# Optimization experiments

Measured on AMD Instinct MI355X. Metric: run time of the kernel, lower is better.

Reference implementation:

```python
import jax, jax.numpy as jnp
import numpy as np

N, M, E = 100000, 500, 300000
XS, GS, OUT, HEADS = 100, 100, 100, 2
SLOPE = 0.2
EPS = 1e-12


def l2norm(x, axis):
    n = jnp.linalg.norm(x, axis=axis, keepdims=True)
    return x / jnp.maximum(n, EPS)


def gat_layer(h_ijk, ends, n, W, att):
    # W: [heads*out, in_dim] (no bias); att: [1, heads, out]
    heads, out = att.shape[1], att.shape[2]
    c = (h_ijk @ W.T).reshape(-1, heads, out)               # [E, H, D]
    a = jnp.sum(att * c, axis=2, keepdims=True)             # [E, H, 1]
    e = jnp.exp(-jax.nn.leaky_relu(a, SLOPE))
    denom = jax.ops.segment_sum(e, ends, num_segments=n)    # [n, H, 1]
    alpha = e / denom[ends]                                 # segment softmax (dropout=eval/identity)
    h = jax.ops.segment_sum(alpha * c, ends, num_segments=n)  # [n, H, D]
    h = jax.nn.elu(h)
    h = l2norm(h, axis=2)
    return h.reshape(n, heads * out)


def merge_layer(h_in, h_out, Wi, bi, Wo, bo, Wl, bl):
    hi = h_in @ Wi.T + bi
    ho = h_out @ Wo.T + bo
    lam = jax.nn.sigmoid(jnp.concatenate([hi, ho], axis=1) @ Wl.T + bl)
    h = lam * hi + (1.0 - lam) * ho
    return l2norm(jax.nn.elu(h), axis=1)


def setup_inputs() -> dict:
    key = jax.random.key(0)
    ks = jax.random.split(key, 24)
    D = HEADS * OUT  # 200
    in1 = 2 * XS + GS   # 300
    in2 = 3 * D         # 600
    s = 0.05
    return {
        'edge_idx': jax.random.randint(ks[0], (2, E), 0, N),
        'edge_type': jax.random.randint(ks[1], (E,), 0, M),
        'path_idx': jax.random.randint(ks[2], (2, 8), 0, N),
        'path_type': jax.random.randint(ks[3], (2, 8), 0, M),
        'use_path': 0,
        'x': jax.random.normal(ks[4], (N, XS), jnp.float32),
        'g': jax.random.normal(ks[5], (M, GS), jnp.float32),
        'W_in1': s * jax.random.normal(ks[6], (D, in1), jnp.float32),
        'att_in1': s * jax.random.normal(ks[7], (1, HEADS, OUT), jnp.float32),
        'W_out1': s * jax.random.normal(ks[8], (D, in1), jnp.float32),
        'att_out1': s * jax.random.normal(ks[9], (1, HEADS, OUT), jnp.float32),
        'Wi1': s * jax.random.normal(ks[10], (D, D), jnp.float32), 'bi1': jnp.zeros((D,), jnp.float32),
        'Wo1': s * jax.random.normal(ks[11], (D, D), jnp.float32), 'bo1': jnp.zeros((D,), jnp.float32),
        'Wl1': s * jax.random.normal(ks[12], (1, 2 * D), jnp.float32), 'bl1': jnp.zeros((1,), jnp.float32),
        'Wr': s * jax.random.normal(ks[13], (D, GS), jnp.float32), 'br': jnp.zeros((D,), jnp.float32),
        'Wf': s * jax.random.normal(ks[14], (D, in1), jnp.float32), 'bf': jnp.zeros((D,), jnp.float32),
        'W_in2': s * jax.random.normal(ks[15], (D, in2), jnp.float32),
        'att_in2': s * jax.random.normal(ks[16], (1, 1, D), jnp.float32),
        'W_out2': s * jax.random.normal(ks[17], (D, in2), jnp.float32),
        'att_out2': s * jax.random.normal(ks[18], (1, 1, D), jnp.float32),
        'Wi2': s * jax.random.normal(ks[19], (D, D), jnp.float32), 'bi2': jnp.zeros((D,), jnp.float32),
        'Wo2': s * jax.random.normal(ks[20], (D, D), jnp.float32), 'bo2': jnp.zeros((D,), jnp.float32),
        'Wl2': s * jax.random.normal(ks[21], (1, 2 * D), jnp.float32), 'bl2': jnp.zeros((1,), jnp.float32),
        'W_ent': s * jax.random.normal(ks[22], (D, XS), jnp.float32),
    }


def reference(edge_idx, edge_type, path_idx, path_type, use_path, x, g,
              W_in1, att_in1, W_out1, att_out1, Wi1, bi1, Wo1, bo1, Wl1, bl1,
              Wr, br, Wf, bf,
              W_in2, att_in2, W_out2, att_out2, Wi2, bi2, Wo2, bo2, Wl2, bl2,
              W_ent):
    n, m = x.shape[0], g.shape[0]
    x = l2norm(x, axis=1)  # x_initial is renormalized each forward
    row, col = edge_idx[0], edge_idx[1]
    # hop 1: gather-concat per-edge features [E, 2*XS+GS]
    h_ijk = jnp.concatenate([x[row], x[col], g[edge_type]], axis=1)
    h_in = gat_layer(h_ijk, col, n, W_in1, att_in1)
    h_out = gat_layer(h_ijk, row, n, W_out1, att_out1)
    h = merge_layer(h_in, h_out, Wi1, bi1, Wo1, bo1, Wl1, bl1)
    # relation layer
    g_edges = jax.ops.segment_sum(h_ijk, edge_type, num_segments=m)
    g_edges = jax.nn.elu(l2norm(g_edges, axis=1))
    g_prime = (g @ Wr.T + br) + (g_edges @ Wf.T + bf)
    # hop 2
    h_ijk2 = jnp.concatenate([h[row], h[col], g_prime[edge_type]], axis=1)
    h_in2 = gat_layer(h_ijk2, col, n, W_in2, att_in2)
    h_out2 = gat_layer(h_ijk2, row, n, W_out2, att_out2)
    h = merge_layer(h_in2, h_out2, Wi2, bi2, Wo2, bo2, Wl2, bl2)
    # entity residual layer
    h_prime = x @ W_ent.T + h
    return h_prime
```

## Files before the change

### kernel.cpp

```cpp
#include <hip/hip_runtime.h>
#include <cstddef>
#include <cstdint>

#define WSLOPE 0.2f
#define WEPS 1e-12f

typedef __attribute__((ext_vector_type(8))) short bf16x8;
typedef __attribute__((ext_vector_type(4))) float f32x4;

__device__ __forceinline__ float waveSum(float v) {
#pragma unroll
    for (int off = 32; off > 0; off >>= 1) v += __shfl_xor(v, off, 64);
    return v;
}
__device__ __forceinline__ float eluf(float v) { return v > 0.f ? v : expm1f(v); }
__device__ __forceinline__ short f2bf(float f) {
    union { float f; uint32_t u; } v; v.f = f;
    uint32_t r = v.u + 0x7FFF + ((v.u >> 16) & 1);
    return (short)(r >> 16);
}

__global__ void k_invnorm(const float* __restrict__ x, float* __restrict__ invn, int N) {
    int wid = blockIdx.x * 4 + (threadIdx.x >> 6);
    int lane = threadIdx.x & 63;
    if (wid >= N) return;
    const float* p = x + (size_t)wid * 100;
    float a = p[lane];
    float ss = a * a;
    if (lane < 36) { float b = p[lane + 64]; ss += b * b; }
    ss = waveSum(ss);
    if (lane == 0) invn[wid] = 1.f / fmaxf(sqrtf(ss), WEPS);
}

__global__ void k_count(const int* __restrict__ keys, int* __restrict__ cnt, int n) {
    int i = blockIdx.x * 256 + threadIdx.x;
    if (i < n) atomicAdd(&cnt[keys[i]], 1);
}

#define SCAN_CHUNK 2048
__global__ void k_blocksum(const int* __restrict__ cnt, int* __restrict__ bsum, int n) {
    __shared__ int sh[256];
    int b = blockIdx.x, t = threadIdx.x;
    int base = b * SCAN_CHUNK;
    int s = 0;
    for (int i = t; i < SCAN_CHUNK; i += 256) { int idx = base + i; if (idx < n) s += cnt[idx]; }
    sh[t] = s; __syncthreads();
    for (int off = 128; off > 0; off >>= 1) { if (t < off) sh[t] += sh[t + off]; __syncthreads(); }
    if (t == 0) bsum[b] = sh[0];
}

__global__ void k_scanwrite(const int* __restrict__ cnt, const int* __restrict__ bsum,
                            int* __restrict__ offs, int* __restrict__ cur, int n, int nb) {
    __shared__ int sh[256];
    __shared__ int sbase;
    int b = blockIdx.x, t = threadIdx.x;
    if (t == 0) { int s = 0; for (int i = 0; i < b; ++i) s += bsum[i]; sbase = s; }
    __syncthreads();
    int base = b * SCAN_CHUNK;
    int loc[8]; int ts = 0;
#pragma unroll
    for (int i = 0; i < 8; ++i) { int idx = base + t * 8 + i; int v = (idx < n) ? cnt[idx] : 0; loc[i] = ts; ts += v; }
    sh[t] = ts; __syncthreads();
    for (int off = 1; off < 256; off <<= 1) {
        int v = (t >= off) ? sh[t - off] : 0;
        __syncthreads();
        sh[t] += v;
        __syncthreads();
    }
    int excl = (t == 0) ? 0 : sh[t - 1];
    int gbase = sbase + excl;
#pragma unroll
    for (int i = 0; i < 8; ++i) {
// ... 44 lines not shown
    int wid = blockIdx.x * 4 + (threadIdx.x >> 6);
    int lane = threadIdx.x & 63;
    if (wid >= N) return;
    if (!HOP2) {
        float inv = invn[wid];
        const float* p = feat + (size_t)wid * 100;
        float f0 = p[lane] * inv;
        float f1 = (lane < 36) ? p[lane + 64] * inv : 0.f;
#pragma unroll
        for (int h = 0; h < 2; ++h) {
            const float* w = wa + h * 300;
            float r = f0 * w[lane] + ((lane < 36) ? f1 * w[lane + 64] : 0.f);
            float c = f0 * w[100 + lane] + ((lane < 36) ? f1 * w[100 + lane + 64] : 0.f);
            r = waveSum(r); c = waveSum(c);
            if (lane == 0) { rdot[wid * 2 + h] = r; cdot[wid * 2 + h] = c; }
        }
    } else {
        const float* p = feat + (size_t)wid * 200;
        float r = 0.f, c = 0.f;
#pragma unroll
        for (int m = 0; m < 4; ++m) {
            int d = lane + m * 64;
            if (d < 200) { float f = p[d]; r += f * wa[d]; c += f * wa[200 + d]; }
        }
        r = waveSum(r); c = waveSum(c);
        if (lane == 0) { rdot[wid] = r; cdot[wid] = c; }
    }
}

__global__ void k_gdot(const float* __restrict__ gsrc, const float* __restrict__ wa,
                       float* __restrict__ gdot, int M, int H, int GL, int K) {
    int id = blockIdx.x * 256 + threadIdx.x;
    if (id >= M * H) return;
    int m = id / H, h = id % H;
    float s = 0.f;
    const float* w = wa + h * K + 2 * GL;
    const float* gm = gsrc + (size_t)m * GL;
    for (int kk = 0; kk < GL; ++kk) s += gm[kk] * w[kk];
    gdot[id] = s;
}

__global__ void k_ew_s(const int* __restrict__ nbrS, const int* __restrict__ keyS,
                       const int* __restrict__ etS,
                       const float* __restrict__ ndot, const float* __restrict__ kdot,
                       const float* __restrict__ gdot, float* __restrict__ ewS, int E, int H) {
    int id = blockIdx.x * 256 + threadIdx.x;
    if (id >= E * H) return;
    int p = id / H, h = id - p * H;
    float a = ndot[nbrS[p] * H + h] + kdot[keyS[p] * H + h] + gdot[etS[p] * H + h];
    float lr = a > 0.f ? a : WSLOPE * a;
    ewS[id] = expf(-lr);
}

template<int H, bool HOP2>
__global__ void k_agg(const int* __restrict__ offs, const int* __restrict__ nbrS,
                      const int* __restrict__ etS, const float* __restrict__ ewS,
                      const float* __restrict__ projg,
                      const float* __restrict__ feat, const float* __restrict__ invn,
                      short* __restrict__ agg_b, float* __restrict__ hb, int n0, int n1) {
    int node = n0 + blockIdx.x * 4 + (threadIdx.x >> 6);
    int lane = threadIdx.x & 63;
    if (node >= n1) return;
    int o = offs[node];
    int deg = offs[node + 1] - o;
    float va[7];
#pragma unroll
    for (int m = 0; m < 7; ++m) va[m] = 0.f;
    if (deg > 0) {
        float s0 = 0.f, s1 = 0.f;
        for (int i = lane; i < deg; i += 64) {
            s0 += ewS[(size_t)(o + i) * H];
            if (H == 2) s1 += ewS[(size_t)(o + i) * H + 1];
        }
        s0 = waveSum(s0);
        float rd0 = 1.f / s0, rd1 = rd0;
        if (H == 2) { s1 = waveSum(s1); rd1 = 1.f / s1; }
        for (int j = 0; j < deg; ++j) {
            float a0 = ewS[(size_t)(o + j) * H] * rd0;
            float a1 = (H == 2) ? ewS[(size_t)(o + j) * H + 1] * rd1 : a0;
            int nbr = nbrS[o + j];
            int et = etS[o + j];
            const float* pgr = projg + (size_t)et * 200;
            if (!HOP2) {
                float inv = invn[nbr];
                const float* fr = feat + (size_t)nbr * 100;
#pragma unroll
                for (int m = 0; m < 7; ++m) {
                    int d = lane + m * 64;
                    if (d < 200) {
                        int kk = d >= 100 ? d - 100 : d;
                        float al = d < 100 ? a0 : a1;
                        va[m] += al * fr[kk] * inv;
                    } else if (d < 400) {
                        int dd = d - 200;
                        float al = dd < 100 ? a0 : a1;
                        va[m] += al * pgr[dd];
                    }
                }
            } else {
                const float* fr = feat + (size_t)nbr * 200;
#pragma unroll
                for (int m = 0; m < 7; ++m) {
                    int d = lane + m * 64;
                    if (d < 200) va[m] += a0 * fr[d];
                    else if (d < 400) va[m] += a0 * pgr[d - 200];
                }
            }
        }
    }
    size_t rb = (size_t)(node - n0);
#pragma unroll
    for (int m = 0; m < 7; ++m) {
        int d = lane + m * 64;
        if (d < 200) {
            int slot = HOP2 ? d : (d < 100 ? d : d + 12);
            agg_b[rb * 224 + slot] = f2bf(va[m]);
        } else if (d < 400) {
            hb[rb * 200 + (d - 200)] = va[m];
        }
    }
    if (!HOP2) {
        if (lane < 24) { int s = lane < 12 ? 100 + lane : 200 + lane; agg_b[rb * 224 + s] = 0; }
    } else {
        if (lane < 24) agg_b[rb * 224 + 200 + lane] = 0;
    }
}

template<int KSTEPS, bool BIAS, bool ACC, bool DEGMASK>
__launch_bounds__(256)
__global__ void k_mgemm(const short* __restrict__ A, const short* __restrict__ Wb,
                        const float* __restrict__ bias, const int* __restrict__ degoffs,
                        float* __restrict__ out, int rows, int lda) {
    constexpr int LDW = KSTEPS * 32;
    const int t = threadIdx.x;
    const int wv = t >> 6, l = t & 63;
    const int lhi = l >> 4, llo = l & 15;
    const int rbase = blockIdx.x * 64 + wv * 16;
    f32x4 acc[13];
#pragma unroll
    for (int j = 0; j < 13; ++j) acc[j] = f32x4{0.f, 0.f, 0.f, 0.f};
    const short* arow = A + (size_t)(rbase + llo) * lda + lhi * 8;
#pragma unroll
    for (int kt = 0; kt < KSTEPS; ++kt) {
        bf16x8 a = *(const bf16x8*)(arow + kt * 32);
#pragma unroll
        for (int j = 0; j < 13; ++j) {
            bf16x8 b = *(const bf16x8*)(Wb + (size_t)(j * 16 + llo) * LDW + kt * 32 + lhi * 8);
            acc[j] = __builtin_amdgcn_mfma_f32_16x16x32_bf16(a, b, acc[j], 0, 0, 0);
        }
    }
    const int r0 = rbase + lhi * 4;
#pragma unroll
    for (int e = 0; e < 4; ++e) {
        int r = r0 + e;
        if (r >= rows) continue;
        float dm = 1.f;
        if (DEGMASK) dm = (degoffs[r + 1] - degoffs[r] == 0) ? 0.f : 1.f;
        float* orow = out + (size_t)r * 200;
#pragma unroll
        for (int j = 0; j < 13; ++j) {
            int d = j * 16 + llo;
            if (d < 200) {
                float v = acc[j][e] * dm;
                if (BIAS) v += bias[d];
                if (ACC) v += orow[d];
                orow[d] = v;
            }
        }
    }
}

__global__ void k_prepw(const float* __restrict__ W, int ldW, int koff, int Klen, int Kpad,
                        int mode, short* __restrict__ Wb) {
    int id = blockIdx.x * 256 + threadIdx.x;
    int tot = 208 * Kpad;
    if (id >= tot) return;
    int d = id / Kpad, k = id - d * Kpad;
    float v = 0.f;
    if (d < 200) {
        if (mode == 0) { if (k < Klen) v = W[(size_t)d * ldW + koff + k]; }
        else { int h = d / 100; int kk = k - h * 112; if (kk >= 0 && kk < 100) v = W[(size_t)d * ldW + koff + kk]; }
    }
    Wb[id] = f2bf(v);
}

__global__ void k_prepwrf(const float* __restrict__ Wr, const float* __restrict__ Wf,
                          short* __restrict__ Wb) {
    int id = blockIdx.x * 256 + threadIdx.x;
    if (id >= 208 * 448) return;
    int d = id / 448, k = id - d * 448;
    float v = 0.f;
    if (d < 200) {
        if (k < 100) v = Wr[(size_t)d * 100 + k];
        else if (k >= 128 && k < 428) v = Wf[(size_t)d * 300 + (k - 128)];
    }
    Wb[id] = f2bf(v);
}

__global__ void k_brf(const float* __restrict__ br, const float* __restrict__ bf,
                      float* __restrict__ brf) {
    int d = threadIdx.x;
    if (d < 200) brf[d] = br[d] + bf[d];
}

__global__ void k_xcb(const float* __restrict__ x, const float* __restrict__ invn,
                      short* __restrict__ sb, int rows) {
    int id = blockIdx.x * 256 + threadIdx.x;
    if (id >= rows * 128) return;
    int r = id >> 7, k = id & 127;
    sb[id] = f2bf(k < 100 ? x[(size_t)r * 100 + k] * invn[r] : 0.f);
}

__global__ void k_gcb(const float* __restrict__ g, short* __restrict__ gb, int rows) {
    int id = blockIdx.x * 256 + threadIdx.x;
    if (id >= rows * 128) return;
    int r = id >> 7, k = id & 127;
    gb[(size_t)r * 448 + k] = f2bf(k < 100 ? g[(size_t)r * 100 + k] : 0.f);
}

__global__ void k_h1b(const float* __restrict__ h1, short* __restrict__ sb, int rows) {
    int id = blockIdx.x * 256 + threadIdx.x;
    if (id >= rows * 224) return;
    int r = id / 224, k = id - r * 224;
    sb[id] = f2bf(k < 200 ? h1[(size_t)r * 200 + k] : 0.f);
}

template<int DH, int H>
__global__ void gat_post2(const float* __restrict__ hb, short* __restrict__ pb, int rowsH) {
    int nh = blockIdx.x * 4 + (threadIdx.x >> 6);
    int lane = threadIdx.x & 63;
    if (nh >= rowsH) return;
    const float* p = hb + (size_t)nh * DH;
    constexpr int MM = (DH + 63) / 64;
    float v[MM];
    float ss = 0.f;
#pragma unroll
    for (int m = 0; m < MM; ++m) {
        int d = lane + m * 64;
        v[m] = 0.f;
        if (d < DH) { v[m] = eluf(p[d]); ss += v[m] * v[m]; }
    }
    ss = waveSum(ss);
    float inv = 1.f / fmaxf(sqrtf(ss), WEPS);
    short* ob = pb + (size_t)(nh / H) * 224 + (size_t)(nh % H) * DH;
#pragma unroll
    for (int m = 0; m < MM; ++m) {
        int d = lane + m * 64;
        if (d < DH) ob[d] = f2bf(v[m] * inv);
    }
}

__global__ void merge_comb(const float* __restrict__ hi, const float* __restrict__ ho,
                           const float* __restrict__ Wl, const float* __restrict__ bl,
                           float* __restrict__ out, int N) {
    int wid = blockIdx.x * 4 + (threadIdx.x >> 6);
    int lane = threadIdx.x & 63;
    if (wid >= N) return;
    float vi[4], vo[4];
    float s = 0.f;
#pragma unroll
    for (int m = 0; m < 4; ++m) {
        int d = lane + m * 64;
        vi[m] = 0.f; vo[m] = 0.f;
        if (d < 200) {
            vi[m] = hi[(size_t)wid * 200 + d];
            vo[m] = ho[(size_t)wid * 200 + d];
            s += Wl[d] * vi[m] + Wl[200 + d] * vo[m];
        }
    }
    s = waveSum(s);
    float lam = 1.f / (1.f + expf(-(s + bl[0])));
    float hv[4];
    float ss = 0.f;
#pragma unroll
    for (int m = 0; m < 4; ++m) {
        int d = lane + m * 64;
        hv[m] = 0.f;
        if (d < 200) {
            float h = lam * vi[m] + (1.f - lam) * vo[m];
            hv[m] = eluf(h);
            ss += hv[m] * hv[m];
        }
    }
    ss = waveSum(ss);
    float inv = 1.f / fmaxf(sqrtf(ss), WEPS);
#pragma unroll
    for (int m = 0; m < 4; ++m) {
        int d = lane + m * 64;
        if (d < 200) out[(size_t)wid * 200 + d] = hv[m] * inv;
    }
}

__global__ void k_gedges_b(const int* __restrict__ rsT, const int* __restrict__ csT,
                           const int* __restrict__ offsT,
                           const float* __restrict__ x, const float* __restrict__ invn,
                           const float* __restrict__ g, short* __restrict__ gcomb, int M) {
    __shared__ float red[4];
    int m = blockIdx.x, t = threadIdx.x;
    int o = offsT[m];
    int deg = offsT[m + 1] - o;
    float acc = 0.f;
    if (t < 100) {
        for (int i = 0; i < deg; ++i) {
            int r = rsT[o + i];
            acc += x[(size_t)r * 100 + t] * invn[r];
        }
    } else if (t < 200) {
        for (int i = 0; i < deg; ++i) {
            int c = csT[o + i];
            acc += x[(size_t)c * 100 + (t - 100)] * invn[c];
        }
    }
    float gval = 0.f;
    if (t < 100) gval = (float)deg * g[(size_t)m * 100 + t];
    float sq = acc * acc + gval * gval;
    sq = waveSum(sq);
    if ((t & 63) == 0) red[t >> 6] = sq;
    __syncthreads();
    float s2 = red[0] + red[1] + red[2] + red[3];
    float inv = 1.f / fmaxf(sqrtf(s2), WEPS);
    short* orow = gcomb + (size_t)m * 448 + 128;
    if (t < 200) orow[t] = f2bf(eluf(acc * inv));
    if (t < 100) orow[200 + t] = f2bf(eluf(gval * inv));
    if (t >= 200 && t < 220) orow[100 + t] = 0;
}

extern "C" void kernel_launch(void* const* d_in, const int* in_sizes, int n_in,
                              void* d_out, int out_size, void* d_ws, size_t ws_size,
                              hipStream_t stream) {
    const int* eidx   = (const int*)d_in[0];
    const int* etype  = (const int*)d_in[1];
    const float* x    = (const float*)d_in[5];
    const float* g    = (const float*)d_in[6];
    const float* W_in1  = (const float*)d_in[7];
    const float* att_in1 = (const float*)d_in[8];
    const float* W_out1 = (const float*)d_in[9];
    const float* att_out1 = (const float*)d_in[10];
    const float* Wi1 = (const float*)d_in[11]; const float* bi1 = (const float*)d_in[12];
    const float* Wo1 = (const float*)d_in[13]; const float* bo1 = (const float*)d_in[14];
    const float* Wl1 = (const float*)d_in[15]; const float* bl1 = (const float*)d_in[16];
    const float* Wr  = (const float*)d_in[17]; const float* br  = (const float*)d_in[18];
    const float* Wf  = (const float*)d_in[19]; const float* bf  = (const float*)d_in[20];
    const float* W_in2  = (const float*)d_in[21]; const float* att_in2 = (const float*)d_in[22];
    const float* W_out2 = (const float*)d_in[23]; const float* att_out2 = (const float*)d_in[24];
    const float* Wi2 = (const float*)d_in[25]; const float* bi2 = (const float*)d_in[26];
    const float* Wo2 = (const float*)d_in[27]; const float* bo2 = (const float*)d_in[28];
    const float* Wl2 = (const float*)d_in[29]; const float* bl2 = (const float*)d_in[30];
    const float* W_ent = (const float*)d_in[31];

    const int E = in_sizes[1];
    const int N = in_sizes[5] / 100;
    const int M = in_sizes[6] / 100;
    const int Mr = (M + 63) & ~63;
    float* out = (float*)d_out;
    const int* row = eidx;
    const int* col = eidx + E;

    char* w = (char*)d_ws;
    size_t off_b = 0;
    auto alloc = [&](size_t bytes) -> void* {
        void* p = w + off_b;
        off_b += (bytes + 255) & ~(size_t)255;
        return p;
    };
    float* invn  = (float*)alloc((size_t)N * 4);
    float* h1    = (float*)alloc((size_t)N * 200 * 4);
    int* offs_in = (int*)alloc((size_t)(N + 1) * 4);
    int* offs_out= (int*)alloc((size_t)(N + 1) * 4);
    int* offsT   = (int*)alloc((size_t)(M + 1) * 4);
    int* nbrS_in = (int*)alloc((size_t)E * 4);
    int* etS_in  = (int*)alloc((size_t)E * 4);
    int* keyS_in = (int*)alloc((size_t)E * 4);
    int* nbrS_out= (int*)alloc((size_t)E * 4);
    int* etS_out = (int*)alloc((size_t)E * 4);
    int* keyS_out= (int*)alloc((size_t)E * 4);
    int* rsT     = (int*)alloc((size_t)E * 4);
    int* csT     = (int*)alloc((size_t)E * 4);
    int* cnt     = (int*)alloc((size_t)N * 4);
    int* cur     = (int*)alloc((size_t)N * 4);
    int* bsum    = (int*)alloc((size_t)64 * 4);
    float* wa_in = (float*)alloc((size_t)1200 * 4);
    float* wa_out= (float*)alloc((size_t)1200 * 4);
    float* rdot_in = (float*)alloc((size_t)N * 2 * 4);
    float* cdot_in = (float*)alloc((size_t)N * 2 * 4);
    float* rdot_out= (float*)alloc((size_t)N * 2 * 4);
    float* cdot_out= (float*)alloc((size_t)N * 2 * 4);
    float* gdot_in = (float*)alloc((size_t)M * 2 * 4);
    float* gdot_out= (float*)alloc((size_t)M * 2 * 4);
    float* ewS_in  = (float*)alloc((size_t)E * 2 * 4);
    float* ewS_out = (float*)alloc((size_t)E * 2 * 4);
    float* pg_in   = (float*)alloc((size_t)M * 200 * 4);
    float* pg_out  = (float*)alloc((size_t)M * 200 * 4);
    float* gp      = (float*)alloc((size_t)M * 200 * 4);
    short* gcomb   = (short*)alloc((size_t)Mr * 448 * 2);
    short* Ws_in1  = (short*)alloc((size_t)208 * 128 * 2);
    short* Ws_out1 = (short*)alloc((size_t)208 * 128 * 2);
    short* Wa_in1  = (short*)alloc((size_t)208 * 224 * 2);
    short* Wa_out1 = (short*)alloc((size_t)208 * 224 * 2);
    short* Wm_i1   = (short*)alloc((size_t)208 * 224 * 2);
    short* Wm_o1   = (short*)alloc((size_t)208 * 224 * 2);
    short* Ws_in2  = (short*)alloc((size_t)208 * 224 * 2);
    short* Ws_out2 = (short*)alloc((size_t)208 * 224 * 2);
    short* Wa_in2  = (short*)alloc((size_t)208 * 224 * 2);
    short* Wa_out2 = (short*)alloc((size_t)208 * 224 * 2);
    short* Wm_i2   = (short*)alloc((size_t)208 * 224 * 2);
    short* Wm_o2   = (short*)alloc((size_t)208 * 224 * 2);
    short* Wb_ent  = (short*)alloc((size_t)208 * 128 * 2);
    short* Wg_in1  = (short*)alloc((size_t)208 * 128 * 2);
    short* Wg_out1 = (short*)alloc((size_t)208 * 128 * 2);
    short* Wg_in2  = (short*)alloc((size_t)208 * 224 * 2);
    short* Wg_out2 = (short*)alloc((size_t)208 * 224 * 2);
    short* Wrf_b   = (short*)alloc((size_t)208 * 448 * 2);
    float* brf     = (float*)alloc((size_t)200 * 4);

    if (off_b >= ws_size) return;
    size_t rem = ws_size - off_b;
    long long Cll = (long long)(rem / 3072);
    long long Nr64 = ((long long)N + 63) & ~63LL;
    int C = (int)(Cll > Nr64 ? Nr64 : Cll);
    C &= ~63;
    if (C < 64) return;
    float* hbA   = (float*)alloc((size_t)C * 200 * 4);
    float* hbB   = (float*)alloc((size_t)C * 200 * 4);
    short* agg_b = (short*)alloc((size_t)C * 224 * 2);
    short* post_b= (short*)alloc((size_t)C * 224 * 2);
    short* sb    = (short*)alloc((size_t)C * 224 * 2);
    if (off_b > ws_size) return;

    const int gE = (E + 255) / 256;
    const int gN4 = (N + 3) / 4;
    const int gM64 = (M + 63) / 64;

    k_invnorm<<<gN4, 256, 0, stream>>>(x, invn, N);

    hipMemsetAsync(post_b, 0, (size_t)C * 224 * 2, stream);

    const int gW224 = (208 * 224 + 255) / 256;
    const int gW128 = (208 * 128 + 255) / 256;
    const int gW448 = (208 * 448 + 255) / 256;
    k_prepw<<<gW128, 256, 0, stream>>>(W_in1, 300, 100, 100, 128, 0, Ws_in1);
    k_prepw<<<gW128, 256, 0, stream>>>(W_out1, 300, 0, 100, 128, 0, Ws_out1);
    k_prepw<<<gW224, 256, 0, stream>>>(W_in1, 300, 0, 100, 224, 1, Wa_in1);
    k_prepw<<<gW224, 256, 0, stream>>>(W_out1, 300, 100, 100, 224, 1, Wa_out1);
    k_prepw<<<gW224, 256, 0, stream>>>(Wi1, 200, 0, 200, 224, 0, Wm_i1);
    k_prepw<<<gW224, 256, 0, stream>>>(Wo1, 200, 0, 200, 224, 0, Wm_o1);
    k_prepw<<<gW224, 256, 0, stream>>>(W_in2, 600, 200, 200, 224, 0, Ws_in2);
    k_prepw<<<gW224, 256, 0, stream>>>(W_out2, 600, 0, 200, 224, 0, Ws_out2);
    k_prepw<<<gW224, 256, 0, stream>>>(W_in2, 600, 0, 200, 224, 0, Wa_in2);
    k_prepw<<<gW224, 256, 0, stream>>>(W_out2, 600, 200, 200, 224, 0, Wa_out2);
    k_prepw<<<gW224, 256, 0, stream>>>(Wi2, 200, 0, 200, 224, 0, Wm_i2);
    k_prepw<<<gW224, 256, 0, stream>>>(Wo2, 200, 0, 200, 224, 0, Wm_o2);
    k_prepw<<<gW128, 256, 0, stream>>>(W_ent, 100, 0, 100, 128, 0, Wb_ent);
    k_prepw<<<gW128, 256, 0, stream>>>(W_in1, 300, 200, 100, 128, 0, Wg_in1);
    k_prepw<<<gW128, 256, 0, stream>>>(W_out1, 300, 200, 100, 128, 0, Wg_out1);
    k_prepw<<<gW224, 256, 0, stream>>>(W_in2, 600, 400, 200, 224, 0, Wg_in2);
    k_prepw<<<gW224, 256, 0, stream>>>(W_out2, 600, 400, 200, 224, 0, Wg_out2);
    k_prepwrf<<<gW448, 256, 0, stream>>>(Wr, Wf, Wrf_b);
    k_brf<<<1, 256, 0, stream>>>(br, bf, brf);

    int nbN = (N + SCAN_CHUNK - 1) / SCAN_CHUNK;
    int nbM = (M + SCAN_CHUNK - 1) / SCAN_CHUNK;
    hipMemsetAsync(cnt, 0, (size_t)N * 4, stream);
    k_count<<<gE, 256, 0, stream>>>(col, cnt, E);
    k_blocksum<<<nbN, 256, 0, stream>>>(cnt, bsum, N);
    k_scanwrite<<<nbN, 256, 0, stream>>>(cnt, bsum, offs_in, cur, N, nbN);
    k_scatter3<<<gE, 256, 0, stream>>>(col, row, etype, cur, nbrS_in, etS_in, keyS_in, E);

    hipMemsetAsync(cnt, 0, (size_t)N * 4, stream);
    k_count<<<gE, 256, 0, stream>>>(row, cnt, E);
    k_blocksum<<<nbN, 256, 0, stream>>>(cnt, bsum, N);
    k_scanwrite<<<nbN, 256, 0, stream>>>(cnt, bsum, offs_out, cur, N, nbN);
    k_scatter3<<<gE, 256, 0, stream>>>(row, col, etype, cur, nbrS_out, etS_out, keyS_out, E);

    hipMemsetAsync(cnt, 0, (size_t)M * 4, stream);
    k_count<<<gE, 256, 0, stream>>>(etype, cnt, E);
    k_blocksum<<<nbM, 256, 0, stream>>>(cnt, bsum, M);
    k_scanwrite<<<nbM, 256, 0, stream>>>(cnt, bsum, offsT, cur, M, nbM);
    k_scatter2<<<gE, 256, 0, stream>>>(etype, cur, rsT, csT, row, col, E);

    k_watt<<<(2 * 300 + 255) / 256, 256, 0, stream>>>(att_in1, W_in1, wa_in, 2, 100, 300);
    k_watt<<<(2 * 300 + 255) / 256, 256, 0, stream>>>(att_out1, W_out1, wa_out, 2, 100, 300);
    k_dots<false><<<gN4, 256, 0, stream>>>(x, invn, wa_in, rdot_in, cdot_in, N);
    k_dots<false><<<gN4, 256, 0, stream>>>(x, invn, wa_out, rdot_out, cdot_out, N);
    k_gdot<<<(M * 2 + 255) / 256, 256, 0, stream>>>(g, wa_in, gdot_in, M, 2, 100, 300);
    k_gdot<<<(M * 2 + 255) / 256, 256, 0, stream>>>(g, wa_out, gdot_out, M, 2, 100, 300);
    k_gcb<<<((int)(((size_t)M * 128 + 255) / 256)), 256, 0, stream>>>(g, gcomb, M);
    k_mgemm<4, false, false, false><<<gM64, 256, 0, stream>>>(gcomb, Wg_in1, nullptr, nullptr, pg_in, M, 448);
    k_mgemm<4, false, false, false><<<gM64, 256, 0, stream>>>(gcomb, Wg_out1, nullptr, nullptr, pg_out, M, 448);
    k_ew_s<<<(E * 2 + 255) / 256, 256, 0, stream>>>(nbrS_in, keyS_in, etS_in, rdot_in, cdot_in, gdot_in, ewS_in, E, 2);
    k_ew_s<<<(E * 2 + 255) / 256, 256, 0, stream>>>(nbrS_out, keyS_out, etS_out, cdot_out, rdot_out, gdot_out, ewS_out, E, 2);

    for (int n0 = 0; n0 < N; n0 += C) {
        int rows = (N - n0 < C) ? (N - n0) : C;
        int n1 = n0 + rows;
        int ga = (rows + 3) / 4;
        int gb = (rows + 63) / 64;
        k_xcb<<<(rows * 128 + 255) / 256, 256, 0, stream>>>(x + (size_t)n0 * 100, invn + n0, sb, rows);
        k_agg<2, false><<<ga, 256, 0, stream>>>(offs_in, nbrS_in, etS_in, ewS_in, pg_in, x, invn, agg_b, hbA, n0, n1);
        k_mgemm<4, false, true, true><<<gb, 256, 0, stream>>>(sb, Ws_in1, nullptr, offs_in + n0, hbA, rows, 128);
        k_mgemm<7, false, true, false><<<gb, 256, 0, stream>>>(agg_b, Wa_in1, nullptr, nullptr, hbA, rows, 224);
        k_agg<2, false><<<ga, 256, 0, stream>>>(offs_out, nbrS_out, etS_out, ewS_out, pg_out, x, invn, agg_b, hbB, n0, n1);
        k_mgemm<4, false, true, true><<<gb, 256, 0, stream>>>(sb, Ws_out1, nullptr, offs_out + n0, hbB, rows, 128);
        k_mgemm<7, false, true, false><<<gb, 256, 0, stream>>>(agg_b, Wa_out1, nullptr, nullptr, hbB, rows, 224);
        gat_post2<100, 2><<<(2 * rows + 3) / 4, 256, 0, stream>>>(hbA, post_b, 2 * rows);
        k_mgemm<7, true, false, false><<<gb, 256, 0, stream>>>(post_b, Wm_i1, bi1, nullptr, hbA, rows, 224);
        gat_post2<100, 2><<<(2 * rows + 3) / 4, 256, 0, stream>>>(hbB, post_b, 2 * rows);
        k_mgemm<7, true, false, false><<<gb, 256, 0, stream>>>(post_b, Wm_o1, bo1, nullptr, hbB, rows, 224);
        merge_comb<<<ga, 256, 0, stream>>>(hbA, hbB, Wl1, bl1, h1 + (size_t)n0 * 200, rows);
    }

    k_gedges_b<<<M, 256, 0, stream>>>(rsT, csT, offsT, x, invn, g, gcomb, M);
    k_mgemm<14, true, false, false><<<gM64, 256, 0, stream>>>(gcomb, Wrf_b, brf, nullptr, gp, M, 448);

    k_watt<<<(600 + 255) / 256, 256, 0, stream>>>(att_in2, W_in2, wa_in, 1, 200, 600);
    k_watt<<<(600 + 255) / 256, 256, 0, stream>>>(att_out2, W_out2, wa_out, 1, 200, 600);
    k_dots<true><<<gN4, 256, 0, stream>>>(h1, nullptr, wa_in, rdot_in, cdot_in, N);
    k_dots<true><<<gN4, 256, 0, stream>>>(h1, nullptr, wa_out, rdot_out, cdot_out, N);
    k_gdot<<<(M + 255) / 256, 256, 0, stream>>>(gp, wa_in, gdot_in, M, 1, 200, 600);
    k_gdot<<<(M + 255) / 256, 256, 0, stream>>>(gp, wa_out, gdot_out, M, 1, 200, 600);
    k_h1b<<<((int)(((size_t)M * 224 + 255) / 256)), 256, 0, stream>>>(gp, gcomb, M);
    k_mgemm<7, false, false, false><<<gM64, 256, 0, stream>>>(gcomb, Wg_in2, nullptr, nullptr, pg_in, M, 224);
    k_mgemm<7, false, false, false><<<gM64, 256, 0, stream>>>(gcomb, Wg_out2, nullptr, nullptr, pg_out, M, 224);
    k_ew_s<<<(E + 255) / 256, 256, 0, stream>>>(nbrS_in, keyS_in, etS_in, rdot_in, cdot_in, gdot_in, ewS_in, E, 1);
    k_ew_s<<<(E + 255) / 256, 256, 0, stream>>>(nbrS_out, keyS_out, etS_out, cdot_out, rdot_out, gdot_out, ewS_out, E, 1);

    for (int n0 = 0; n0 < N; n0 += C) {
        int rows = (N - n0 < C) ? (N - n0) : C;
        int n1 = n0 + rows;
        int ga = (rows + 3) / 4;
        int gb = (rows + 63) / 64;
        k_h1b<<<(rows * 224 + 255) / 256, 256, 0, stream>>>(h1 + (size_t)n0 * 200, sb, rows);
        k_agg<1, true><<<ga, 256, 0, stream>>>(offs_in, nbrS_in, etS_in, ewS_in, pg_in, h1, nullptr, agg_b, hbA, n0, n1);
        k_mgemm<7, false, true, true><<<gb, 256, 0, stream>>>(sb, Ws_in2, nullptr, offs_in + n0, hbA, rows, 224);
        k_mgemm<7, false, true, false><<<gb, 256, 0, stream>>>(agg_b, Wa_in2, nullptr, nullptr, hbA, rows, 224);
        k_agg<1, true><<<ga, 256, 0, stream>>>(offs_out, nbrS_out, etS_out, ewS_out, pg_out, h1, nullptr, agg_b, hbB, n0, n1);
        k_mgemm<7, false, true, true><<<gb, 256, 0, stream>>>(sb, Ws_out2, nullptr, offs_out + n0, hbB, rows, 224);
        k_mgemm<7, false, true, false><<<gb, 256, 0, stream>>>(agg_b, Wa_out2, nullptr, nullptr, hbB, rows, 224);
        gat_post2<200, 1><<<ga, 256, 0, stream>>>(hbA, post_b, rows);
        k_mgemm<7, true, false, false><<<gb, 256, 0, stream>>>(post_b, Wm_i2, bi2, nullptr, hbA, rows, 224);
        gat_post2<200, 1><<<ga, 256, 0, stream>>>(hbB, post_b, rows);
        k_mgemm<7, true, false, false><<<gb, 256, 0, stream>>>(post_b, Wm_o2, bo2, nullptr, hbB, rows, 224);
        merge_comb<<<ga, 256, 0, stream>>>(hbA, hbB, Wl2, bl2, out + (size_t)n0 * 200, rows);
        k_xcb<<<(rows * 128 + 255) / 256, 256, 0, stream>>>(x + (size_t)n0 * 100, invn + n0, sb, rows);
        k_mgemm<4, false, true, false><<<gb, 256, 0, stream>>>(sb, Wb_ent, nullptr, nullptr, out + (size_t)n0 * 200, rows, 128);
    }
}
```

Before: 2.958 ms.

## Fuse GAT projections into single concatenated-K GEMM over bf16 aggregated features

The aggregation kernel now gathers bf16 node and relation features, skipping the per-relation projected tables, and writes one wide A row per node holding the aggregated node features, aggregated relation features and the masked self features. A single MFMA GEMM with concatenated weights (K=576 or 672) then replaces the three separate GEMMs and the relation pre-projection GEMMs. Node features are pre-converted to bf16 once, and merge_comb emits a bf16 copy of h1 for hop 2. This removes several kernel launches and repeated fp32 read-modify-write passes over the output buffers. In exchange it adds more bf16 rounding of gathered features and a larger per-row A buffer, which shrinks the chunk size.

```diff
diff --git a/kernel.cpp b/kernel.cpp
--- a/kernel.cpp
+++ b/kernel.cpp
@@ -18,6 +18,10 @@
     union { float f; uint32_t u; } v; v.f = f;
     uint32_t r = v.u + 0x7FFF + ((v.u >> 16) & 1);
     return (short)(r >> 16);
+}
+__device__ __forceinline__ float bf2f(short s) {
+    union { uint32_t u; float f; } v; v.u = ((uint32_t)(uint16_t)s) << 16;
+    return v.f;
 }
 
 __global__ void k_invnorm(const float* __restrict__ x, float* __restrict__ invn, int N) {
@@ -168,12 +172,15 @@
     ewS[id] = expf(-lr);
 }
 
-template<int H, bool HOP2>
+template<bool HOP2>
 __global__ void k_agg(const int* __restrict__ offs, const int* __restrict__ nbrS,
                       const int* __restrict__ etS, const float* __restrict__ ewS,
-                      const float* __restrict__ projg,
-                      const float* __restrict__ feat, const float* __restrict__ invn,
-                      short* __restrict__ agg_b, float* __restrict__ hb, int n0, int n1) {
+                      const short* __restrict__ featB, const short* __restrict__ gB,
+                      short* __restrict__ A, int n0, int n1) {
+    constexpr int H = HOP2 ? 1 : 2;
+    constexpr int LDA = HOP2 ? 672 : 576;
+    constexpr int FW = HOP2 ? 224 : 112;
+    constexpr int GW = HOP2 ? 224 : 112;
     int node = n0 + blockIdx.x * 4 + (threadIdx.x >> 6);
     int lane = threadIdx.x & 63;
     if (node >= n1) return;
@@ -196,56 +203,65 @@
             float a1 = (H == 2) ? ewS[(size_t)(o + j) * H + 1] * rd1 : a0;
             int nbr = nbrS[o + j];
             int et = etS[o + j];
-            const float* pgr = projg + (size_t)et * 200;
+            const short* fr = featB + (size_t)nbr * FW;
+            const short* gr = gB + (size_t)et * GW;
             if (!HOP2) {
-                float inv = invn[nbr];
-                const float* fr = feat + (size_t)nbr * 100;
 #pragma unroll
                 for (int m = 0; m < 7; ++m) {
                     int d = lane + m * 64;
-                    if (d < 200) {
-                        int kk = d >= 100 ? d - 100 : d;
-                        float al = d < 100 ? a0 : a1;
-                        va[m] += al * fr[kk] * inv;
-                    } else if (d < 400) {
-                        int dd = d - 200;
-                        float al = dd < 100 ? a0 : a1;
-                        va[m] += al * pgr[dd];
-                    }
+                    if (d < 100) va[m] += a0 * bf2f(fr[d]);
+                    else if (d < 200) va[m] += a1 * bf2f(fr[d - 100]);
+                    else if (d < 300) va[m] += a0 * bf2f(gr[d - 200]);
+                    else if (d < 400) va[m] += a1 * bf2f(gr[d - 300]);
                 }
             } else {
-                const float* fr = feat + (size_t)nbr * 200;
 #pragma unroll
                 for (int m = 0; m < 7; ++m) {
                     int d = lane + m * 64;
-                    if (d < 200) va[m] += a0 * fr[d];
-                    else if (d < 400) va[m] += a0 * pgr[d - 200];
+                    if (d < 200) va[m] += a0 * bf2f(fr[d]);
+                    else if (d < 424) va[m] += a0 * bf2f(gr[d - 200]);
                 }
             }
         }
     }
     size_t rb = (size_t)(node - n0);
-#pragma unroll
-    for (int m = 0; m < 7; ++m) {
-        int d = lane + m * 64;
-        if (d < 200) {
-            int slot = HOP2 ? d : (d < 100 ? d : d + 12);
-            agg_b[rb * 224 + slot] = f2bf(va[m]);
-        } else if (d < 400) {
-            hb[rb * 200 + (d - 200)] = va[m];
-        }
-    }
+    short* Ar = A + rb * LDA;
     if (!HOP2) {
-        if (lane < 24) { int s = lane < 12 ? 100 + lane : 200 + lane; agg_b[rb * 224 + s] = 0; }
+#pragma unroll
+        for (int m = 0; m < 7; ++m) {
+            int d = lane + m * 64;
+            if (d < 400) {
+                int col = d < 100 ? d : (d < 200 ? d + 12 : (d < 300 ? d + 24 : d + 36));
+                Ar[col] = f2bf(va[m]);
+            }
+        }
+        if (lane < 48) { int q = lane / 12; int rm = lane - q * 12; Ar[q * 112 + 100 + rm] = 0; }
+        const short* sf = featB + (size_t)node * 112;
+#pragma unroll
+        for (int mm = 0; mm < 2; ++mm) {
+            int k = lane + mm * 64;
+            if (k < 128) Ar[448 + k] = (deg > 0 && k < 112) ? sf[k] : (short)0;
+        }
     } else {
-        if (lane < 24) agg_b[rb * 224 + 200 + lane] = 0;
-    }
-}
-
-template<int KSTEPS, bool BIAS, bool ACC, bool DEGMASK>
+#pragma unroll
+        for (int m = 0; m < 7; ++m) {
+            int d = lane + m * 64;
+            if (d < 424) Ar[d < 200 ? d : d + 24] = f2bf(va[m]);
+        }
+        if (lane < 24) Ar[200 + lane] = 0;
+        const short* sf = featB + (size_t)node * 224;
+#pragma unroll
+        for (int mm = 0; mm < 4; ++mm) {
+            int k = lane + mm * 64;
+            if (k < 224) Ar[448 + k] = deg > 0 ? sf[k] : (short)0;
+        }
+    }
+}
+
+template<int KSTEPS, bool BIAS, bool ACC>
 __launch_bounds__(256)
 __global__ void k_mgemm(const short* __restrict__ A, const short* __restrict__ Wb,
-                        const float* __restrict__ bias, const int* __restrict__ degoffs,
+                        const float* __restrict__ bias,
                         float* __restrict__ out, int rows, int lda) {
     constexpr int LDW = KSTEPS * 32;
     const int t = threadIdx.x;
@@ -270,14 +286,12 @@
     for (int e = 0; e < 4; ++e) {
         int r = r0 + e;
         if (r >= rows) continue;
-        float dm = 1.f;
-        if (DEGMASK) dm = (degoffs[r + 1] - degoffs[r] == 0) ? 0.f : 1.f;
         float* orow = out + (size_t)r * 200;
 #pragma unroll
         for (int j = 0; j < 13; ++j) {
             int d = j * 16 + llo;
             if (d < 200) {
-                float v = acc[j][e] * dm;
+                float v = acc[j][e];
                 if (BIAS) v += bias[d];
                 if (ACC) v += orow[d];
                 orow[d] = v;
@@ -286,18 +300,18 @@
     }
 }
 
-__global__ void k_prepw(const float* __restrict__ W, int ldW, int koff, int Klen, int Kpad,
-                        int mode, short* __restrict__ Wb) {
-    int id = blockIdx.x * 256 + threadIdx.x;
-    int tot = 208 * Kpad;
+__global__ void k_prepw(const float* __restrict__ W, int ldW, int koff, int Klen, int span,
+                        int mode, short* __restrict__ Wb, int ldWb, int dst) {
+    int id = blockIdx.x * 256 + threadIdx.x;
+    int tot = 208 * span;
     if (id >= tot) return;
-    int d = id / Kpad, k = id - d * Kpad;
+    int d = id / span, k = id - d * span;
     float v = 0.f;
     if (d < 200) {
         if (mode == 0) { if (k < Klen) v = W[(size_t)d * ldW + koff + k]; }
-        else { int h = d / 100; int kk = k - h * 112; if (kk >= 0 && kk < 100) v = W[(size_t)d * ldW + koff + kk]; }
-    }
-    Wb[id] = f2bf(v);
+        else { int h = d / 100; int kk = k - h * 112; if (kk >= 0 && kk < Klen) v = W[(size_t)d * ldW + koff + kk]; }
+    }
+    Wb[(size_t)d * ldWb + dst + k] = f2bf(v);
 }
 
 __global__ void k_prepwrf(const float* __restrict__ Wr, const float* __restrict__ Wf,
@@ -319,12 +333,14 @@
     if (d < 200) brf[d] = br[d] + bf[d];
 }
 
-__global__ void k_xcb(const float* __restrict__ x, const float* __restrict__ invn,
-                      short* __restrict__ sb, int rows) {
-    int id = blockIdx.x * 256 + threadIdx.x;
-    if (id >= rows * 128) return;
-    int r = id >> 7, k = id & 127;
-    sb[id] = f2bf(k < 100 ? x[(size_t)r * 100 + k] * invn[r] : 0.f);
+__global__ void k_cvt112(const float* __restrict__ src, const float* __restrict__ invn,
+                         short* __restrict__ dst, int rows) {
+    int id = blockIdx.x * 256 + threadIdx.x;
+    if (id >= rows * 112) return;
+    int r = id / 112, k = id - r * 112;
+    float v = 0.f;
+    if (k < 100) { v = src[(size_t)r * 100 + k]; if (invn) v *= invn[r]; }
+    dst[id] = f2bf(v);
 }
 
 __global__ void k_gcb(const float* __restrict__ g, short* __restrict__ gb, int rows) {
@@ -368,7 +384,7 @@
 
 __global__ void merge_comb(const float* __restrict__ hi, const float* __restrict__ ho,
                            const float* __restrict__ Wl, const float* __restrict__ bl,
-                           float* __restrict__ out, int N) {
+                           float* __restrict__ out, short* __restrict__ hbf, int N) {
     int wid = blockIdx.x * 4 + (threadIdx.x >> 6);
     int lane = threadIdx.x & 63;
     if (wid >= N) return;
@@ -403,7 +419,13 @@
 #pragma unroll
     for (int m = 0; m < 4; ++m) {
         int d = lane + m * 64;
-        if (d < 200) out[(size_t)wid * 200 + d] = hv[m] * inv;
+        if (d < 200) {
+            float v = hv[m] * inv;
+            out[(size_t)wid * 200 + d] = v;
+            if (hbf) hbf[(size_t)wid * 224 + d] = f2bf(v);
+        } else if (d < 224) {
+            if (hbf) hbf[(size_t)wid * 224 + d] = 0;
+        }
     }
 }
 
@@ -411,34 +433,43 @@
                            const int* __restrict__ offsT,
                            const float* __restrict__ x, const float* __restrict__ invn,
                            const float* __restrict__ g, short* __restrict__ gcomb, int M) {
-    __shared__ float red[4];
+    __shared__ float red[6];
     int m = blockIdx.x, t = threadIdx.x;
     int o = offsT[m];
     int deg = offsT[m + 1] - o;
     float acc = 0.f;
-    if (t < 100) {
+    if (t < 128) {
+        int d = t; bool ok = d < 100;
         for (int i = 0; i < deg; ++i) {
             int r = rsT[o + i];
-            acc += x[(size_t)r * 100 + t] * invn[r];
-        }
-    } else if (t < 200) {
+            if (ok) acc += x[(size_t)r * 100 + d] * invn[r];
+        }
+    } else if (t < 256) {
+        int d = t - 128; bool ok = d < 100;
         for (int i = 0; i < deg; ++i) {
             int c = csT[o + i];
-            acc += x[(size_t)c * 100 + (t - 100)] * invn[c];
-        }
-    }
-    float gval = 0.f;
-    if (t < 100) gval = (float)deg * g[(size_t)m * 100 + t];
-    float sq = acc * acc + gval * gval;
-    sq = waveSum(sq);
+            if (ok) acc += x[(size_t)c * 100 + d] * invn[c];
+        }
+    } else {
+        int d = t - 256;
+        if (d < 100) acc = (float)deg * g[(size_t)m * 100 + d];
+    }
+    float sq = waveSum(acc * acc);
     if ((t & 63) == 0) red[t >> 6] = sq;
     __syncthreads();
-    float s2 = red[0] + red[1] + red[2] + red[3];
+    float s2 = red[0] + red[1] + red[2] + red[3] + red[4] + red[5];
     float inv = 1.f / fmaxf(sqrtf(s2), WEPS);
     short* orow = gcomb + (size_t)m * 448 + 128;
-    if (t < 200) orow[t] = f2bf(eluf(acc * inv));
-    if (t < 100) orow[200 + t] = f2bf(eluf(gval * inv));
-    if (t >= 200 && t < 220) orow[100 + t] = 0;
+    if (t < 128) {
+        if (t < 100) orow[t] = f2bf(eluf(acc * inv));
+    } else if (t < 256) {
+        int d = t - 128;
+        if (d < 100) orow[100 + d] = f2bf(eluf(acc * inv));
+    } else {
+        int d = t - 256;
+        if (d < 100) orow[200 + d] = f2bf(eluf(acc * inv));
+        else if (d < 120) orow[200 + d] = 0;
+    }
 }
 
 extern "C" void kernel_launch(void* const* d_in, const int* in_sizes, int n_in,
@@ -481,6 +512,9 @@
     };
     float* invn  = (float*)alloc((size_t)N * 4);
     float* h1    = (float*)alloc((size_t)N * 200 * 4);
+    short* h1_bf = (short*)alloc((size_t)(N + 64) * 224 * 2);
+    short* xn_bf = (short*)alloc((size_t)(N + 64) * 112 * 2);
+    short* g_bf  = (short*)alloc((size_t)M * 112 * 2);
     int* offs_in = (int*)alloc((size_t)(N + 1) * 4);
     int* offs_out= (int*)alloc((size_t)(N + 1) * 4);
     int* offsT   = (int*)alloc((size_t)(M + 1) * 4);
@@ -505,42 +539,31 @@
     float* gdot_out= (float*)alloc((size_t)M * 2 * 4);
     float* ewS_in  = (float*)alloc((size_t)E * 2 * 4);
     float* ewS_out = (float*)alloc((size_t)E * 2 * 4);
-    float* pg_in   = (float*)alloc((size_t)M * 200 * 4);
-    float* pg_out  = (float*)alloc((size_t)M * 200 * 4);
     float* gp      = (float*)alloc((size_t)M * 200 * 4);
     short* gcomb   = (short*)alloc((size_t)Mr * 448 * 2);
-    short* Ws_in1  = (short*)alloc((size_t)208 * 128 * 2);
-    short* Ws_out1 = (short*)alloc((size_t)208 * 128 * 2);
-    short* Wa_in1  = (short*)alloc((size_t)208 * 224 * 2);
-    short* Wa_out1 = (short*)alloc((size_t)208 * 224 * 2);
+    short* Wc_in1  = (short*)alloc((size_t)208 * 576 * 2);
+    short* Wc_out1 = (short*)alloc((size_t)208 * 576 * 2);
+    short* Wc_in2  = (short*)alloc((size_t)208 * 672 * 2);
+    short* Wc_out2 = (short*)alloc((size_t)208 * 672 * 2);
     short* Wm_i1   = (short*)alloc((size_t)208 * 224 * 2);
     short* Wm_o1   = (short*)alloc((size_t)208 * 224 * 2);
-    short* Ws_in2  = (short*)alloc((size_t)208 * 224 * 2);
-    short* Ws_out2 = (short*)alloc((size_t)208 * 224 * 2);
-    short* Wa_in2  = (short*)alloc((size_t)208 * 224 * 2);
-    short* Wa_out2 = (short*)alloc((size_t)208 * 224 * 2);
     short* Wm_i2   = (short*)alloc((size_t)208 * 224 * 2);
     short* Wm_o2   = (short*)alloc((size_t)208 * 224 * 2);
     short* Wb_ent  = (short*)alloc((size_t)208 * 128 * 2);
-    short* Wg_in1  = (short*)alloc((size_t)208 * 128 * 2);
-    short* Wg_out1 = (short*)alloc((size_t)208 * 128 * 2);
-    short* Wg_in2  = (short*)alloc((size_t)208 * 224 * 2);
-    short* Wg_out2 = (short*)alloc((size_t)208 * 224 * 2);
     short* Wrf_b   = (short*)alloc((size_t)208 * 448 * 2);
     float* brf     = (float*)alloc((size_t)200 * 4);
 
     if (off_b >= ws_size) return;
     size_t rem = ws_size - off_b;
-    long long Cll = (long long)(rem / 3072);
+    long long Cll = (long long)(rem / 3520);
     long long Nr64 = ((long long)N + 63) & ~63LL;
     int C = (int)(Cll > Nr64 ? Nr64 : Cll);
     C &= ~63;
     if (C < 64) return;
     float* hbA   = (float*)alloc((size_t)C * 200 * 4);
     float* hbB   = (float*)alloc((size_t)C * 200 * 4);
-    short* agg_b = (short*)alloc((size_t)C * 224 * 2);
+    short* Ac    = (short*)alloc((size_t)C * 672 * 2);
     short* post_b= (short*)alloc((size_t)C * 224 * 2);
-    short* sb    = (short*)alloc((size_t)C * 224 * 2);
     if (off_b > ws_size) return;
 
     const int gE = (E + 255) / 256;
@@ -551,27 +574,28 @@
 
     hipMemsetAsync(post_b, 0, (size_t)C * 224 * 2, stream);
 
-    const int gW224 = (208 * 224 + 255) / 256;
-    const int gW128 = (208 * 128 + 255) / 256;
-    const int gW448 = (208 * 448 + 255) / 256;
-    k_prepw<<<gW128, 256, 0, stream>>>(W_in1, 300, 100, 100, 128, 0, Ws_in1);
-    k_prepw<<<gW128, 256, 0, stream>>>(W_out1, 300, 0, 100, 128, 0, Ws_out1);
-    k_prepw<<<gW224, 256, 0, stream>>>(W_in1, 300, 0, 100, 224, 1, Wa_in1);
-    k_prepw<<<gW224, 256, 0, stream>>>(W_out1, 300, 100, 100, 224, 1, Wa_out1);
-    k_prepw<<<gW224, 256, 0, stream>>>(Wi1, 200, 0, 200, 224, 0, Wm_i1);
-    k_prepw<<<gW224, 256, 0, stream>>>(Wo1, 200, 0, 200, 224, 0, Wm_o1);
-    k_prepw<<<gW224, 256, 0, stream>>>(W_in2, 600, 200, 200, 224, 0, Ws_in2);
-    k_prepw<<<gW224, 256, 0, stream>>>(W_out2, 600, 0, 200, 224, 0, Ws_out2);
-    k_prepw<<<gW224, 256, 0, stream>>>(W_in2, 600, 0, 200, 224, 0, Wa_in2);
-    k_prepw<<<gW224, 256, 0, stream>>>(W_out2, 600, 200, 200, 224, 0, Wa_out2);
-    k_prepw<<<gW224, 256, 0, stream>>>(Wi2, 200, 0, 200, 224, 0, Wm_i2);
-    k_prepw<<<gW224, 256, 0, stream>>>(Wo2, 200, 0, 200, 224, 0, Wm_o2);
-    k_prepw<<<gW128, 256, 0, stream>>>(W_ent, 100, 0, 100, 128, 0, Wb_ent);
-    k_prepw<<<gW128, 256, 0, stream>>>(W_in1, 300, 200, 100, 128, 0, Wg_in1);
-    k_prepw<<<gW128, 256, 0, stream>>>(W_out1, 300, 200, 100, 128, 0, Wg_out1);
-    k_prepw<<<gW224, 256, 0, stream>>>(W_in2, 600, 400, 200, 224, 0, Wg_in2);
-    k_prepw<<<gW224, 256, 0, stream>>>(W_out2, 600, 400, 200, 224, 0, Wg_out2);
-    k_prepwrf<<<gW448, 256, 0, stream>>>(Wr, Wf, Wrf_b);
+    k_cvt112<<<((int)(((size_t)N * 112 + 255) / 256)), 256, 0, stream>>>(x, invn, xn_bf, N);
+    k_cvt112<<<((int)(((size_t)M * 112 + 255) / 256)), 256, 0, stream>>>(g, nullptr, g_bf, M);
+
+    auto gsp = [](int span) { return (208 * span + 255) / 256; };
+    k_prepw<<<gsp(224), 256, 0, stream>>>(W_in1, 300, 0, 100, 224, 1, Wc_in1, 576, 0);
+    k_prepw<<<gsp(224), 256, 0, stream>>>(W_in1, 300, 200, 100, 224, 1, Wc_in1, 576, 224);
+    k_prepw<<<gsp(128), 256, 0, stream>>>(W_in1, 300, 100, 100, 128, 0, Wc_in1, 576, 448);
+    k_prepw<<<gsp(224), 256, 0, stream>>>(W_out1, 300, 100, 100, 224, 1, Wc_out1, 576, 0);
+    k_prepw<<<gsp(224), 256, 0, stream>>>(W_out1, 300, 200, 100, 224, 1, Wc_out1, 576, 224);
+    k_prepw<<<gsp(128), 256, 0, stream>>>(W_out1, 300, 0, 100, 128, 0, Wc_out1, 576, 448);
+    k_prepw<<<gsp(224), 256, 0, stream>>>(W_in2, 600, 0, 200, 224, 0, Wc_in2, 672, 0);
+    k_prepw<<<gsp(224), 256, 0, stream>>>(W_in2, 600, 400, 200, 224, 0, Wc_in2, 672, 224);
+    k_prepw<<<gsp(224), 256, 0, stream>>>(W_in2, 600, 200, 200, 224, 0, Wc_in2, 672, 448);
+    k_prepw<<<gsp(224), 256, 0, stream>>>(W_out2, 600, 200, 200, 224, 0, Wc_out2, 672, 0);
+    k_prepw<<<gsp(224), 256, 0, stream>>>(W_out2, 600, 400, 200, 224, 0, Wc_out2, 672, 224);
+    k_prepw<<<gsp(224), 256, 0, stream>>>(W_out2, 600, 0, 200, 224, 0, Wc_out2, 672, 448);
+    k_prepw<<<gsp(224), 256, 0, stream>>>(Wi1, 200, 0, 200, 224, 0, Wm_i1, 224, 0);
+    k_prepw<<<gsp(224), 256, 0, stream>>>(Wo1, 200, 0, 200, 224, 0, Wm_o1, 224, 0);
+    k_prepw<<<gsp(224), 256, 0, stream>>>(Wi2, 200, 0, 200, 224, 0, Wm_i2, 224, 0);
+    k_prepw<<<gsp(224), 256, 0, stream>>>(Wo2, 200, 0, 200, 224, 0, Wm_o2, 224, 0);
+    k_prepw<<<gsp(128), 256, 0, stream>>>(W_ent, 100, 0, 100, 128, 0, Wb_ent, 128, 0);
+    k_prepwrf<<<gsp(448), 256, 0, stream>>>(Wr, Wf, Wrf_b);
     k_brf<<<1, 256, 0, stream>>>(br, bf, brf);
 
     int nbN = (N + SCAN_CHUNK - 1) / SCAN_CHUNK;
@@ -600,33 +624,29 @@
     k_dots<false><<<gN4, 256, 0, stream>>>(x, invn, wa_out, rdot_out, cdot_out, N);
     k_gdot<<<(M * 2 + 255) / 256, 256, 0, stream>>>(g, wa_in, gdot_in, M, 2, 100, 300);
     k_gdot<<<(M * 2 + 255) / 256, 256, 0, stream>>>(g, wa_out, gdot_out, M, 2, 100, 300);
-    k_gcb<<<((int)(((size_t)M * 128 + 255) / 256)), 256, 0, stream>>>(g, gcomb, M);
-    k_mgemm<4, false, false, false><<<gM64, 256, 0, stream>>>(gcomb, Wg_in1, nullptr, nullptr, pg_in, M, 448);
-    k_mgemm<4, false, false, false><<<gM64, 256, 0, stream>>>(gcomb, Wg_out1, nullptr, nullptr, pg_out, M, 448);
     k_ew_s<<<(E * 2 + 255) / 256, 256, 0, stream>>>(nbrS_in, keyS_in, etS_in, rdot_in, cdot_in, gdot_in, ewS_in, E, 2);
     k_ew_s<<<(E * 2 + 255) / 256, 256, 0, stream>>>(nbrS_out, keyS_out, etS_out, cdot_out, rdot_out, gdot_out, ewS_out, E, 2);
+    k_gcb<<<((int)(((size_t)M * 128 + 255) / 256)), 256, 0, stream>>>(g, gcomb, M);
 
     for (int n0 = 0; n0 < N; n0 += C) {
         int rows = (N - n0 < C) ? (N - n0) : C;
         int n1 = n0 + rows;
         int ga = (rows + 3) / 4;
         int gb = (rows + 63) / 64;
-        k_xcb<<<(rows * 128 + 255) / 256, 256, 0, stream>>>(x + (size_t)n0 * 100, invn + n0, sb, rows);
-        k_agg<2, false><<<ga, 256, 0, stream>>>(offs_in, nbrS_in, etS_in, ewS_in, pg_in, x, invn, agg_b, hbA, n0, n1);
-        k_mgemm<4, false, true, true><<<gb, 256, 0, stream>>>(sb, Ws_in1, nullptr, offs_in + n0, hbA, rows, 128);
-        k_mgemm<7, false, true, false><<<gb, 256, 0, stream>>>(agg_b, Wa_in1, nullptr, nullptr, hbA, rows, 224);
-        k_agg<2, false><<<ga, 256, 0, stream>>>(offs_out, nbrS_out, etS_out, ewS_out, pg_out, x, invn, agg_b, hbB, n0, n1);
-        k_mgemm<4, false, true, true><<<gb, 256, 0, stream>>>(sb, Ws_out1, nullptr, offs_out + n0, hbB, rows, 128);
-        k_mgemm<7, false, true, false><<<gb, 256, 0, stream>>>(agg_b, Wa_out1, nullptr, nullptr, hbB, rows, 224);
+        k_agg<false><<<ga, 256, 0, stream>>>(offs_in, nbrS_in, etS_in, ewS_in, xn_bf, g_bf, Ac, n0, n1);
+        k_mgemm<18, false, false><<<gb, 256, 0, stream>>>(Ac, Wc_in1, nullptr, hbA, rows, 576);
         gat_post2<100, 2><<<(2 * rows + 3) / 4, 256, 0, stream>>>(hbA, post_b, 2 * rows);
-        k_mgemm<7, true, false, false><<<gb, 256, 0, stream>>>(post_b, Wm_i1, bi1, nullptr, hbA, rows, 224);
+        k_mgemm<7, true, false><<<gb, 256, 0, stream>>>(post_b, Wm_i1, bi1, hbA, rows, 224);
+        k_agg<false><<<ga, 256, 0, stream>>>(offs_out, nbrS_out, etS_out, ewS_out, xn_bf, g_bf, Ac, n0, n1);
+        k_mgemm<18, false, false><<<gb, 256, 0, stream>>>(Ac, Wc_out1, nullptr, hbB, rows, 576);
         gat_post2<100, 2><<<(2 * rows + 3) / 4, 256, 0, stream>>>(hbB, post_b, 2 * rows);
-        k_mgemm<7, true, false, false><<<gb, 256, 0, stream>>>(post_b, Wm_o1, bo1, nullptr, hbB, rows, 224);
-        merge_comb<<<ga, 256, 0, stream>>>(hbA, hbB, Wl1, bl1, h1 + (size_t)n0 * 200, rows);
-    }
-
-    k_gedges_b<<<M, 256, 0, stream>>>(rsT, csT, offsT, x, invn, g, gcomb, M);
-    k_mgemm<14, true, false, false><<<gM64, 256, 0, stream>>>(gcomb, Wrf_b, brf, nullptr, gp, M, 448);
+        k_mgemm<7, true, false><<<gb, 256, 0, stream>>>(post_b, Wm_o1, bo1, hbB, rows, 224);
+        merge_comb<<<ga, 256, 0, stream>>>(hbA, hbB, Wl1, bl1, h1 + (size_t)n0 * 200,
+                                           h1_bf + (size_t)n0 * 224, rows);
+    }
+
+    k_gedges_b<<<M, 384, 0, stream>>>(rsT, csT, offsT, x, invn, g, gcomb, M);
+    k_mgemm<14, true, false><<<gM64, 256, 0, stream>>>(gcomb, Wrf_b, brf, gp, M, 448);
 
     k_watt<<<(600 + 255) / 256, 256, 0, stream>>>(att_in2, W_in2, wa_in, 1, 200, 600);
     k_watt<<<(600 + 255) / 256, 256, 0, stream>>>(att_out2, W_out2, wa_out, 1, 200, 600);
@@ -635,8 +655,6 @@
     k_gdot<<<(M + 255) / 256, 256, 0, stream>>>(gp, wa_in, gdot_in, M, 1, 200, 600);
     k_gdot<<<(M + 255) / 256, 256, 0, stream>>>(gp, wa_out, gdot_out, M, 1, 200, 600);
     k_h1b<<<((int)(((size_t)M * 224 + 255) / 256)), 256, 0, stream>>>(gp, gcomb, M);
-    k_mgemm<7, false, false, false><<<gM64, 256, 0, stream>>>(gcomb, Wg_in2, nullptr, nullptr, pg_in, M, 224);
-    k_mgemm<7, false, false, false><<<gM64, 256, 0, stream>>>(gcomb, Wg_out2, nullptr, nullptr, pg_out, M, 224);
     k_ew_s<<<(E + 255) / 256, 256, 0, stream>>>(nbrS_in, keyS_in, etS_in, rdot_in, cdot_in, gdot_in, ewS_in, E, 1);
     k_ew_s<<<(E + 255) / 256, 256, 0, stream>>>(nbrS_out, keyS_out, etS_out, cdot_out, rdot_out, gdot_out, ewS_out, E, 1);
 
@@ -645,19 +663,16 @@
         int n1 = n0 + rows;
         int ga = (rows + 3) / 4;
         int gb = (rows + 63) / 64;
-        k_h1b<<<(rows * 224 + 255) / 256, 256, 0, stream>>>(h1 + (size_t)n0 * 200, sb, rows);
-        k_agg<1, true><<<ga, 256, 0, stream>>>(offs_in, nbrS_in, etS_in, ewS_in, pg_in, h1, nullptr, agg_b, hbA, n0, n1);
-        k_mgemm<7, false, true, true><<<gb, 256, 0, stream>>>(sb, Ws_in2, nullptr, offs_in + n0, hbA, rows, 224);
-        k_mgemm<7, false, true, false><<<gb, 256, 0, stream>>>(agg_b, Wa_in2, nullptr, nullptr, hbA, rows, 224);
-        k_agg<1, true><<<ga, 256, 0, stream>>>(offs_out, nbrS_out, etS_out, ewS_out, pg_out, h1, nullptr, agg_b, hbB, n0, n1);
-        k_mgemm<7, false, true, true><<<gb, 256, 0, stream>>>(sb, Ws_out2, nullptr, offs_out + n0, hbB, rows, 224);
-        k_mgemm<7, false, true, false><<<gb, 256, 0, stream>>>(agg_b, Wa_out2, nullptr, nullptr, hbB, rows, 224);
+        k_agg<true><<<ga, 256, 0, stream>>>(offs_in, nbrS_in, etS_in, ewS_in, h1_bf, gcomb, Ac, n0, n1);
+        k_mgemm<21, false, false><<<gb, 256, 0, stream>>>(Ac, Wc_in2, nullptr, hbA, rows, 672);
         gat_post2<200, 1><<<ga, 256, 0, stream>>>(hbA, post_b, rows);
-        k_mgemm<7, true, false, false><<<gb, 256, 0, stream>>>(post_b, Wm_i2, bi2, nullptr, hbA, rows, 224);
+        k_mgemm<7, true, false><<<gb, 256, 0, stream>>>(post_b, Wm_i2, bi2, hbA, rows, 224);
+        k_agg<true><<<ga, 256, 0, stream>>>(offs_out, nbrS_out, etS_out, ewS_out, h1_bf, gcomb, Ac, n0, n1);
+        k_mgemm<21, false, false><<<gb, 256, 0, stream>>>(Ac, Wc_out2, nullptr, hbB, rows, 672);
         gat_post2<200, 1><<<ga, 256, 0, stream>>>(hbB, post_b, rows);
-        k_mgemm<7, true, false, false><<<gb, 256, 0, stream>>>(post_b, Wm_o2, bo2, nullptr, hbB, rows, 224);
-        merge_comb<<<ga, 256, 0, stream>>>(hbA, hbB, Wl2, bl2, out + (size_t)n0 * 200, rows);
-        k_xcb<<<(rows * 128 + 255) / 256, 256, 0, stream>>>(x + (size_t)n0 * 100, invn + n0, sb, rows);
-        k_mgemm<4, false, true, false><<<gb, 256, 0, stream>>>(sb, Wb_ent, nullptr, nullptr, out + (size_t)n0 * 200, rows, 128);
-    }
-}
+        k_mgemm<7, true, false><<<gb, 256, 0, stream>>>(post_b, Wm_o2, bo2, hbB, rows, 224);
+        merge_comb<<<ga, 256, 0, stream>>>(hbA, hbB, Wl2, bl2, out + (size_t)n0 * 200, nullptr, rows);
+        k_mgemm<4, false, true><<<gb, 256, 0, stream>>>(xn_bf + (size_t)n0 * 112, Wb_ent, nullptr,
+                                                        out + (size_t)n0 * 200, rows, 112);
+    }
+}
```

After: 2.887 ms. 1.02x faster.
